# Kernel optimization log

Hardware: AMD Instinct MI355X
Metric: run time of the kernel (lower is better)

Reference implementation:

```python
import jax, jax.numpy as jnp
import numpy as np

T, B, IN_DIM, HID, ACT = 512, 256, 256, 256, 16


def _dense_params(key, din, dout, scale=0.02):
    kw, _ = jax.random.split(key)
    return jax.random.normal(kw, (din, dout), jnp.float32) * scale, jnp.zeros((dout,), jnp.float32)


def setup_inputs() -> dict:
    key = jax.random.key(0)
    ks = jax.random.split(key, 12)
    x = jax.random.normal(ks[0], (T, B, IN_DIM), jnp.float32)
    dones = jax.random.bernoulli(ks[1], 0.05, (T, B))
    h0_c = jnp.zeros((B, HID), jnp.float32)
    h0_h = jnp.zeros((B, HID), jnp.float32)
    W_embed, b_embed = _dense_params(ks[2], IN_DIM, HID)
    # OptimizedLSTMCell: fused gate projections, gate order (i, f, g, o)
    Wi = jax.random.normal(ks[3], (HID, 4 * HID), jnp.float32) * 0.02
    Wh = jax.random.normal(ks[4], (HID, 4 * HID), jnp.float32) * 0.02
    b_lstm = jnp.zeros((4 * HID,), jnp.float32)
    Wa1, ba1 = _dense_params(ks[5], HID, HID // 2)
    Wa2, ba2 = _dense_params(ks[6], HID // 2, HID // 2)
    Wa3, ba3 = _dense_params(ks[7], HID // 2, ACT, scale=0.01)
    Wc1, bc1 = _dense_params(ks[8], HID, HID // 2)
    Wc2, bc2 = _dense_params(ks[9], HID // 2, HID // 2)
    Wc3, bc3 = _dense_params(ks[10], HID // 2, 1)
    return dict(x=x, dones=dones, h0_c=h0_c, h0_h=h0_h,
                W_embed=W_embed, b_embed=b_embed, Wi=Wi, Wh=Wh, b_lstm=b_lstm,
                Wa1=Wa1, ba1=ba1, Wa2=Wa2, ba2=ba2, Wa3=Wa3, ba3=ba3,
                Wc1=Wc1, bc1=bc1, Wc2=Wc2, bc2=bc2, Wc3=Wc3, bc3=bc3)


def reference(x, dones, h0_c, h0_h, W_embed, b_embed, Wi, Wh, b_lstm,
              Wa1, ba1, Wa2, ba2, Wa3, ba3, Wc1, bc1, Wc2, bc2, Wc3, bc3):
    # embed (note: source overwrites first Dense; effective embed is one Dense+relu)
    embed = jax.nn.relu(jnp.einsum('tbi,ih->tbh', x, W_embed) + b_embed)

    def step(carry, inp):
        c, h = carry
        xt, rt = inp  # xt: [B, HID], rt: [B] bool
        m = rt[:, None]
        c = jnp.where(m, 0.0, c)  # reset_carry is zeros (initialize_carry)
        h = jnp.where(m, 0.0, h)
        z = xt @ Wi + h @ Wh + b_lstm  # [B, 4*HID]
        i, f, g, o = jnp.split(z, 4, axis=-1)
        c_new = jax.nn.sigmoid(f) * c + jax.nn.sigmoid(i) * jnp.tanh(g)
        h_new = jax.nn.sigmoid(o) * jnp.tanh(c_new)
        return (c_new, h_new), h_new

    (c_fin, h_fin), hs = jax.lax.scan(step, (h0_c, h0_h), (embed, dones))

    a = jnp.tanh(jnp.einsum('tbh,hk->tbk', hs, Wa1) + ba1)
    a = jnp.tanh(a @ Wa2 + ba2)
    logits = a @ Wa3 + ba3  # [T, B, ACT]

    v = jnp.tanh(jnp.einsum('tbh,hk->tbk', hs, Wc1) + bc1)
    v = jnp.tanh(v @ Wc2 + bc2)
    value = jnp.squeeze(v @ Wc3 + bc3, axis=-1)  # [T, B]

    return c_fin, h_fin, logits, value
```

## Files before the change

kernel.cpp:

```cpp
#include <hip/hip_runtime.h>
#include <stdint.h>


typedef short v8s __attribute__((ext_vector_type(8)));
typedef float v4f __attribute__((ext_vector_type(4)));

#define DEV static __device__ __forceinline__
#define DT_THRESH 4096

DEV float b2f(unsigned short h) {
    union { unsigned int u; float f; } v; v.u = ((unsigned int)h) << 16; return v.f;
}
DEV unsigned short f2b(float f) {
    union { float f; unsigned int u; } v; v.f = f;
    unsigned int u = v.u;
    return (unsigned short)((u + 0x7fffu + ((u >> 16) & 1u)) >> 16);
}
DEV float sigf(float x) {
    x = fminf(fmaxf(x, -30.f), 30.f);
    return 1.f / (1.f + __expf(-x));
}
DEV float tanh_(float x) {
    x = fminf(fmaxf(x, -15.f), 15.f);
    float e = __expf(-2.f * x);
    return (1.f - e) / (1.f + e);
}

__global__ __launch_bounds__(1024) void dones_k(const void* __restrict__ raw,
                                                int* __restrict__ dst,
                                                int* __restrict__ dt) {
    __shared__ int bad_int, bad_bf;
    int tid = threadIdx.x;
    if (tid == 0) { bad_int = 0; bad_bf = 0; dt[0] = 0; }
    __syncthreads();
    const unsigned int* w = (const unsigned int*)raw;
    int li = 0, lb = 0;
    for (int i = tid; i < 32768; i += 1024) {
        unsigned int v = w[i];
        if (v > 1u) li = 1;
        unsigned int h0 = v & 0xffffu, h1 = v >> 16;
        if ((h0 != 0u && h0 != 0x3f80u) || (h1 != 0u && h1 != 0x3f80u)) lb = 1;
    }
    if (li) atomicOr(&bad_int, 1);
    if (lb) atomicOr(&bad_bf, 1);
    __syncthreads();
    int mode = (!bad_int) ? 0 : ((!bad_bf) ? 1 : 2);
    for (int e = tid; e < 131072; e += 1024) {
        int v;
        if (mode == 0)      v = (((const int*)raw)[e] != 0);
        else if (mode == 1) v = (((const unsigned short*)raw)[e] != 0);
        else                v = (((const unsigned char*)raw)[e] != 0);
        dst[e] = v;
    }
}

__global__ __launch_bounds__(256) void detect_k(const unsigned short* __restrict__ xr,
                                                int* __restrict__ dt) {
    int tid = blockIdx.x * 256 + threadIdx.x;
    int cnt = 0;
    for (int i = tid; i < (1 << 24); i += 16384) {
        unsigned int e = (xr[i] >> 7) & 0xffu;
        cnt += (e >= 140u);
    }
    for (int o = 32; o; o >>= 1) cnt += __shfl_down(cnt, o);
    if ((threadIdx.x & 63) == 0 && cnt) atomicAdd(dt, cnt);
}

__global__ __launch_bounds__(256) void cvt_x_k(const void* __restrict__ xr,
                                               unsigned short* __restrict__ xb,
                                               const int* __restrict__ dt) {
    int fp32i = dt[0] > DT_THRESH;
    long i4 = (long)blockIdx.x * 256 + threadIdx.x;
    if (fp32i) {
        float4 v = ((const float4*)xr)[i4];
        uint2 p;
        p.x = (unsigned int)f2b(v.x) | ((unsigned int)f2b(v.y) << 16);
        p.y = (unsigned int)f2b(v.z) | ((unsigned int)f2b(v.w) << 16);
        ((uint2*)xb)[i4] = p;
    } else {
        ((uint2*)xb)[i4] = ((const uint2*)xr)[i4];
    }
}

struct TransArgs {
    const void* src[9];
    unsigned short* dst[9];
    int R[9];
    int C[9];
    int prefix[10];
    int total;
};

__global__ __launch_bounds__(256) void trans_kernel(TransArgs a, const int* __restrict__ dt) {
    int fp32i = dt[0] > DT_THRESH;
    int id = blockIdx.x * 256 + threadIdx.x;
    if (id >= a.total) return;
    int m = 0;
#pragma unroll
    for (int k = 0; k < 9; k++)
        if (id >= a.prefix[k + 1]) m = k + 1;
    int e = id - a.prefix[m];
    int C = a.C[m];
    int r = e / C, c = e % C;
    unsigned short v;
    if (fp32i) v = f2b(((const float*)a.src[m])[e]);
    else       v = ((const unsigned short*)a.src[m])[e];
    a.dst[m][c * a.R[m] + r] = v;
}

template <int TN, int ACT, int OM>
__global__ __launch_bounds__(256) void gemm_k(const unsigned short* __restrict__ A,
                                              const unsigned short* __restrict__ BT,
                                              const unsigned short* __restrict__ bias,
                                              void* __restrict__ Cout, long coff,
                                              const int* __restrict__ dtf,
                                              int N, int K) {
    __shared__ unsigned short As[128][40];
    __shared__ unsigned short Bs[TN][40];
    const int tid = threadIdx.x;
    const int l = tid & 63, w = tid >> 6;
    const long m0 = (long)blockIdx.x * 128;
    const int n0 = blockIdx.y * TN;
    constexpr int NRT = (TN == 128) ? 4 : 2;
    constexpr int NCT = (TN == 128) ? 4 : 1;
    int fp32o = (OM == 1) ? (dtf[0] > DT_THRESH) : 0;

    v4f acc[NRT][NCT];
    for (int i = 0; i < NRT; i++)
        for (int j = 0; j < NCT; j++) acc[i][j] = v4f{0.f, 0.f, 0.f, 0.f};

    for (int kc = 0; kc < K; kc += 32) {
        {
            int row = tid >> 1, part = tid & 1;
            const uint4* src = (const uint4*)(A + (m0 + row) * K + kc + part * 16);
            uint4 v0 = src[0], v1 = src[1];
            *(uint4*)&As[row][part * 16] = v0;
            *(uint4*)&As[row][part * 16 + 8] = v1;
        }
        if (TN == 128) {
            int row = tid >> 1, part = tid & 1;
            const uint4* src = (const uint4*)(BT + (long)(n0 + row) * K + kc + part * 16);
            uint4 v0 = src[0], v1 = src[1];
            *(uint4*)&Bs[row][part * 16] = v0;
            *(uint4*)&Bs[row][part * 16 + 8] = v1;
        } else if (tid < 32) {
            int row = tid >> 1, part = tid & 1;
            const uint4* src = (const uint4*)(BT + (long)(n0 + row) * K + kc + part * 16);
            uint4 v0 = src[0], v1 = src[1];
            *(uint4*)&Bs[row][part * 16] = v0;
            *(uint4*)&Bs[row][part * 16 + 8] = v1;
        }
        __syncthreads();

        v8s af[NRT], bf[NCT];
#pragma unroll
        for (int i = 0; i < NRT; i++) {
            int rt = (TN == 128) ? ((w >> 1) * 4 + i) : (w * 2 + i);
            af[i] = *(const v8s*)&As[rt * 16 + (l & 15)][(l >> 4) * 8];
        }
#pragma unroll
        for (int j = 0; j < NCT; j++) {
            int ct = (TN == 128) ? ((w & 1) * 4 + j) : 0;
            bf[j] = *(const v8s*)&Bs[ct * 16 + (l & 15)][(l >> 4) * 8];
        }
#pragma unroll
        for (int i = 0; i < NRT; i++)
#pragma unroll
            for (int j = 0; j < NCT; j++)
                acc[i][j] = __builtin_amdgcn_mfma_f32_16x16x32_bf16(af[i], bf[j], acc[i][j], 0, 0, 0);
        __syncthreads();
    }

#pragma unroll
    for (int j = 0; j < NCT; j++) {
        int ct = (TN == 128) ? ((w & 1) * 4 + j) : 0;
        int col = ct * 16 + (l & 15);
        float bv = b2f(bias[n0 + col]);
#pragma unroll
        for (int i = 0; i < NRT; i++) {
            int rt = (TN == 128) ? ((w >> 1) * 4 + i) : (w * 2 + i);
#pragma unroll
            for (int q = 0; q < 4; q++) {
                long row = m0 + rt * 16 + (l >> 4) * 4 + q;
                float v = acc[i][j][q] + bv;
                if (ACT == 1) v = fmaxf(v, 0.f);
                if (ACT == 2) v = tanh_(v);
                long idx = coff + row * (long)N + n0 + col;
                if (OM == 1 && fp32o) ((float*)Cout)[idx] = v;
                else ((unsigned short*)Cout)[idx] = f2b(v);
            }
        }
    }
}

#define HB_WORDS 65536

__global__ __launch_bounds__(512, 2) void lstm_k(const unsigned short* __restrict__ xz,
                                                 const int* __restrict__ dones,
                                                 const void* __restrict__ h0c,
                                                 const void* __restrict__ h0h,
                                                 const unsigned short* __restrict__ WhT,
                                                 unsigned int* __restrict__ hb,
                                                 unsigned short* __restrict__ hs,
                                                 void* __restrict__ outv,
                                                 const int* __restrict__ dtf) {
    __shared__ unsigned short hlds[16][256];
    __shared__ float zlds[4][16][132];

    const int tid = threadIdx.x;
    const int l = tid & 63;
    const int w = tid >> 6;
    const int cluster = blockIdx.x & 15;
    const int r = blockIdx.x >> 4;
    const int p = r ^ 1;
    const int bt = cluster * 16;
    const int fp32o = dtf[0] > DT_THRESH;
    const int gate = w & 3;
    const int hblk = (w >> 2) * 64;
    const int l15 = l & 15;
    const int lq = l >> 4;

    v8s bw[4][8];
#pragma unroll
    for (int j = 0; j < 4; j++) {
        const unsigned short* wp =
            WhT + (long)(gate * 256 + r * 128 + hblk + j * 16 + l15) * 256 + lq * 8;
#pragma unroll
        for (int ks = 0; ks < 8; ks++) bw[j][ks] = *(const v8s*)(wp + ks * 32);
    }

    float c[4], hcur[4] = {0.f, 0.f, 0.f, 0.f};
#pragma unroll
    for (int i = 0; i < 4; i++) {
        int cell = i * 512 + tid;
        int row = cell >> 7, hid = cell & 127;
        long idx = (long)(bt + row) * 256 + r * 128 + hid;
        c[i] = fp32o ? ((const float*)h0c)[idx] : b2f(((const unsigned short*)h0c)[idx]);
        float h0 = fp32o ? ((const float*)h0h)[idx] : b2f(((const unsigned short*)h0h)[idx]);
        unsigned short hbits = f2b(h0);
        hlds[row][(r * 128 + hid) ^ ((row & 7) * 8)] = hbits;
        __hip_atomic_store(&hb[(size_t)cluster * 4096 + row * 256 + r * 128 + hid],
                           (unsigned int)hbits,
                           __ATOMIC_RELAXED, __HIP_MEMORY_SCOPE_AGENT);
    }

    int dead = 0;
    unsigned int va[4] = {0u, 0u, 0u, 0u};

    for (int t = 0; t < 512; t++) {
        unsigned short xzp[16];
#pragma unroll
        for (int j = 0; j < 4; j++)
#pragma unroll
            for (int q = 0; q < 4; q++)
                xzp[j * 4 + q] = xz[(long)(t * 256 + bt + lq * 4 + q) * 1024 +
                                    (gate * 256 + r * 128 + hblk + j * 16 + l15)];
        int dn_a = dones[t * 256 + bt + l15];
        int dn_c[4];
#pragma unroll
        for (int i = 0; i < 4; i++) dn_c[i] = dones[t * 256 + bt + i * 4 + (tid >> 7)];

        const unsigned int tag = (unsigned int)t;
        const unsigned int* rb = hb + (size_t)(t & 1) * HB_WORDS + (size_t)cluster * 4096;
        if (!dead) {
            int guard = 0;
            while (true) {
#pragma unroll
                for (int i = 0; i < 4; i++) {
                    int cell = i * 512 + tid;
                    va[i] = __hip_atomic_load(&rb[(cell >> 7) * 256 + p * 128 + (cell & 127)],
                                              __ATOMIC_RELAXED, __HIP_MEMORY_SCOPE_AGENT);
                }
                unsigned int okl = ((va[0] >> 16) == tag) & ((va[1] >> 16) == tag) &
                                   ((va[2] >> 16) == tag) & ((va[3] >> 16) == tag);
                if (__ballot(okl != 0u) == ~0ull) break;
                if (++guard > (1 << 13)) { dead = 1; break; }
            }
        }
#pragma unroll
        for (int i = 0; i < 4; i++) {
            int cell = i * 512 + tid;
            int row = cell >> 7, hid = cell & 127;
            hlds[row][(p * 128 + hid) ^ ((row & 7) * 8)] = (unsigned short)(va[i] & 0xffffu);
        }
        __syncthreads();

        v4f acc[4];
#pragma unroll
        for (int j = 0; j < 4; j++)
#pragma unroll
            for (int q = 0; q < 4; q++) acc[j][q] = b2f(xzp[j * 4 + q]);
#pragma unroll
        for (int ks = 0; ks < 8; ks++) {
            v8s a = *(const v8s*)&hlds[l15][(ks * 32 + lq * 8) ^ ((l15 & 7) * 8)];
            if (dn_a) a = v8s{0, 0, 0, 0, 0, 0, 0, 0};
#pragma unroll
            for (int j = 0; j < 4; j++)
                acc[j] = __builtin_amdgcn_mfma_f32_16x16x32_bf16(a, bw[j][ks], acc[j], 0, 0, 0);
        }
#pragma unroll
        for (int j = 0; j < 4; j++)
#pragma unroll
            for (int q = 0; q < 4; q++)
                zlds[gate][lq * 4 + q][hblk + j * 16 + l15] = acc[j][q];
        __syncthreads();

        unsigned int* wb = hb + (size_t)((t + 1) & 1) * HB_WORDS + (size_t)cluster * 4096;
#pragma unroll
        for (int i = 0; i < 4; i++) {
            int cell = i * 512 + tid;
            int row = cell >> 7, hid = cell & 127;
            float zi = zlds[0][row][hid];
            float zf = zlds[1][row][hid];
            float zg = zlds[2][row][hid];
            float zo = zlds[3][row][hid];
            float cm = dn_c[i] ? 0.f : c[i];
            float cn = sigf(zf) * cm + sigf(zi) * tanh_(zg);
            float h = sigf(zo) * tanh_(cn);
            c[i] = cn;
            hcur[i] = h;
            unsigned short hbits = f2b(h);
            hlds[row][(r * 128 + hid) ^ ((row & 7) * 8)] = hbits;
            __hip_atomic_store(&wb[row * 256 + r * 128 + hid],
                               (((unsigned int)(t + 1)) << 16) | (unsigned int)hbits,
                               __ATOMIC_RELAXED, __HIP_MEMORY_SCOPE_AGENT);
            unsigned int pr = (unsigned int)__shfl_xor((int)hbits, 1);
            if ((tid & 1) == 0) {
                unsigned int wv = (unsigned int)hbits | (pr << 16);
                ((unsigned int*)hs)[((long)(t * 256 + bt + row)) * 128 + ((r * 128 + hid) >> 1)] = wv;
            }
        }
    }

#pragma unroll
    for (int i = 0; i < 4; i++) {
        int cell = i * 512 + tid;
        int row = cell >> 7, hid = cell & 127;
        long i1 = (long)(bt + row) * 256 + r * 128 + hid;
        long i2 = 65536 + i1;
        if (fp32o) {
            ((float*)outv)[i1] = c[i];
            ((float*)outv)[i2] = hcur[i];
        } else {
            ((unsigned short*)outv)[i1] = f2b(c[i]);
            ((unsigned short*)outv)[i2] = f2b(hcur[i]);
        }
    }
}

__global__ __launch_bounds__(256) void value_k(const unsigned short* __restrict__ V2,
                                               const unsigned short* __restrict__ Wc3T,
                                               const unsigned short* __restrict__ bc3,
                                               void* __restrict__ outv,
                                               const int* __restrict__ dtf) {
    int tid = threadIdx.x;
    int l = tid & 63, w = tid >> 6;
    int fp32o = dtf[0] > DT_THRESH;
    long row = (long)blockIdx.x * 32 + w * 8 + (l >> 3);
    int sub = l & 7;
    const unsigned short* vp = V2 + row * 128 + sub * 16;
    float s = 0.f;
#pragma unroll
    for (int j = 0; j < 16; j++) s += b2f(vp[j]) * b2f(Wc3T[sub * 16 + j]);
    s += __shfl_xor(s, 1);
    s += __shfl_xor(s, 2);
    s += __shfl_xor(s, 4);
    if (sub == 0) {
        float v = s + b2f(bc3[0]);
        if (fp32o) ((float*)outv)[2228224 + row] = v;
        else ((unsigned short*)outv)[2228224 + row] = f2b(v);
    }
}

extern "C" void kernel_launch(void* const* d_in, const int* in_sizes, int n_in,
                              void* d_out, int out_size, void* d_ws, size_t ws_size,
                              hipStream_t stream) {
    const void* x             = d_in[0];
    const void* dones_raw     = d_in[1];
    const void* h0c           = d_in[2];
    const void* h0h           = d_in[3];
    const void* We  = d_in[4];
    const unsigned short* be  = (const unsigned short*)d_in[5];
    const void* Wi  = d_in[6];
    const void* Wh  = d_in[7];
    const unsigned short* bl  = (const unsigned short*)d_in[8];
    const void* Wa1 = d_in[9];
    const unsigned short* ba1 = (const unsigned short*)d_in[10];
    const void* Wa2 = d_in[11];
    const unsigned short* ba2 = (const unsigned short*)d_in[12];
    const void* Wa3 = d_in[13];
    const unsigned short* ba3 = (const unsigned short*)d_in[14];
    const void* Wc1 = d_in[15];
    const unsigned short* bc1 = (const unsigned short*)d_in[16];
    const void* Wc2 = d_in[17];
    const unsigned short* bc2 = (const unsigned short*)d_in[18];
    const void* Wc3 = d_in[19];
    const unsigned short* bc3 = (const unsigned short*)d_in[20];
    char* ws = (char*)d_ws;

    unsigned short* WeT  = (unsigned short*)(ws + 0);
    unsigned short* WiT  = (unsigned short*)(ws + 131072);
    unsigned short* WhT  = (unsigned short*)(ws + 655360);
    unsigned short* Wa1T = (unsigned short*)(ws + 1179648);
    unsigned short* Wa2T = (unsigned short*)(ws + 1245184);
    unsigned short* Wa3T = (unsigned short*)(ws + 1277952);
    unsigned short* Wc1T = (unsigned short*)(ws + 1282048);
    unsigned short* Wc2T = (unsigned short*)(ws + 1347584);
    unsigned short* Wc3T = (unsigned short*)(ws + 1380352);
    int*            DT   = (int*)(ws + 1380608);
    unsigned int*   HB   = (unsigned int*)(ws + 1380672);
    int*            DN   = (int*)(ws + 1904960);
    unsigned short* XB   = (unsigned short*)(ws + 2429248);
    unsigned short* E    = (unsigned short*)(ws + 69538112);
    unsigned short* XZ   = (unsigned short*)(ws + 136646976);
    unsigned short* HS   = (unsigned short*)(ws + 405082432);
    unsigned short* H1   = XB;
    unsigned short* H2   = XB + 16777216;

    TransArgs ta;
    {
        const void* srcs[9] = {We, Wi, Wh, Wa1, Wa2, Wa3, Wc1, Wc2, Wc3};
        unsigned short* dsts[9] = {WeT, WiT, WhT, Wa1T, Wa2T, Wa3T, Wc1T, Wc2T, Wc3T};
        int Rs[9] = {256, 256, 256, 256, 128, 128, 256, 128, 128};
        int Cs[9] = {256, 1024, 1024, 128, 128, 16, 128, 128, 1};
        int p = 0;
        for (int i = 0; i < 9; i++) {
            ta.src[i] = srcs[i];
            ta.dst[i] = dsts[i];
            ta.R[i] = Rs[i];
            ta.C[i] = Cs[i];
            ta.prefix[i] = p;
            p += Rs[i] * Cs[i];
        }
        ta.prefix[9] = p;
        ta.total = p;
    }

    dones_k<<<1, 1024, 0, stream>>>(dones_raw, DN, DT);
    detect_k<<<64, 256, 0, stream>>>((const unsigned short*)x, DT);
    cvt_x_k<<<32768, 256, 0, stream>>>(x, XB, DT);
    trans_kernel<<<2697, 256, 0, stream>>>(ta, DT);

    gemm_k<128, 1, 0><<<dim3(1024, 2), 256, 0, stream>>>(XB, WeT, be, E, 0, nullptr, 256, 256);
    gemm_k<128, 0, 0><<<dim3(1024, 8), 256, 0, stream>>>(E, WiT, bl, XZ, 0, nullptr, 1024, 256);
    lstm_k<<<32, 512, 0, stream>>>(XZ, DN, h0c, h0h, WhT, HB, HS, d_out, DT);
    gemm_k<128, 2, 0><<<dim3(1024, 1), 256, 0, stream>>>(HS, Wa1T, ba1, H1, 0, nullptr, 128, 256);
    gemm_k<128, 2, 0><<<dim3(1024, 1), 256, 0, stream>>>(H1, Wa2T, ba2, H2, 0, nullptr, 128, 128);
    gemm_k<16, 0, 1><<<dim3(1024, 1), 256, 0, stream>>>(H2, Wa3T, ba3, d_out, 131072, DT, 16, 128);
    gemm_k<128, 2, 0><<<dim3(1024, 1), 256, 0, stream>>>(HS, Wc1T, bc1, H1, 0, nullptr, 128, 256);
    gemm_k<128, 2, 0><<<dim3(1024, 1), 256, 0, stream>>>(H1, Wc2T, bc2, H2, 0, nullptr, 128, 128);
    value_k<<<4096, 256, 0, stream>>>(H2, Wc3T, bc3, d_out, DT);
}
```

Measured before the change: 2.657 ms.

## Replace per-element tagged handoff with flag-based release/acquire and overlap local half

The LSTM recurrence swaps tagged per-element polling of the partner block's h values for a single release/acquire flag per block, with h packed as bf16 pairs in a double-buffered exchange area. The MFMA for the block's own half of h now runs before waiting on the partner, so part of the matmul overlaps the cross-block sync. Next-step xz gate inputs and dones are prefetched one step ahead, and the done mask is applied when h is produced, not at the MFMA input. Per-thread cell mapping becomes four contiguous hidden units, enabling vectorised LDS, global and hs stores, at the cost of an extra __syncthreads per step and a flag-initialisation dependency in dones_k.

```diff
diff --git a/kernel.cpp b/kernel.cpp
--- a/kernel.cpp
+++ b/kernel.cpp
@@ -4,6 +4,7 @@
 
 typedef short v8s __attribute__((ext_vector_type(8)));
 typedef float v4f __attribute__((ext_vector_type(4)));
+typedef unsigned short u16x4 __attribute__((ext_vector_type(4)));
 
 #define DEV static __device__ __forceinline__
 #define DT_THRESH 4096
@@ -28,10 +29,12 @@
 
 __global__ __launch_bounds__(1024) void dones_k(const void* __restrict__ raw,
                                                 int* __restrict__ dst,
-                                                int* __restrict__ dt) {
+                                                int* __restrict__ dt,
+                                                unsigned int* __restrict__ flg) {
     __shared__ int bad_int, bad_bf;
     int tid = threadIdx.x;
     if (tid == 0) { bad_int = 0; bad_bf = 0; dt[0] = 0; }
+    for (int i = tid; i < 2048; i += 1024) flg[i] = 0u;
     __syncthreads();
     const unsigned int* w = (const unsigned int*)raw;
     int li = 0, lb = 0;
@@ -193,14 +196,13 @@
     }
 }
 
-#define HB_WORDS 65536
-
 __global__ __launch_bounds__(512, 2) void lstm_k(const unsigned short* __restrict__ xz,
                                                  const int* __restrict__ dones,
                                                  const void* __restrict__ h0c,
                                                  const void* __restrict__ h0h,
                                                  const unsigned short* __restrict__ WhT,
-                                                 unsigned int* __restrict__ hb,
+                                                 unsigned int* __restrict__ flg,
+                                                 unsigned int* __restrict__ hd32,
                                                  unsigned short* __restrict__ hs,
                                                  void* __restrict__ outv,
                                                  const int* __restrict__ dtf) {
@@ -219,6 +221,9 @@
     const int hblk = (w >> 2) * 64;
     const int l15 = l & 15;
     const int lq = l >> 4;
+    const int row = tid >> 5;
+    const int hid0 = (tid & 31) * 4;
+    const int swz = (row & 7) * 8;
 
     v8s bw[4][8];
 #pragma unroll
@@ -230,70 +235,89 @@
     }
 
     float c[4], hcur[4] = {0.f, 0.f, 0.f, 0.f};
-#pragma unroll
-    for (int i = 0; i < 4; i++) {
-        int cell = i * 512 + tid;
-        int row = cell >> 7, hid = cell & 127;
-        long idx = (long)(bt + row) * 256 + r * 128 + hid;
-        c[i] = fp32o ? ((const float*)h0c)[idx] : b2f(((const unsigned short*)h0c)[idx]);
-        float h0 = fp32o ? ((const float*)h0h)[idx] : b2f(((const unsigned short*)h0h)[idx]);
-        unsigned short hbits = f2b(h0);
-        hlds[row][(r * 128 + hid) ^ ((row & 7) * 8)] = hbits;
-        __hip_atomic_store(&hb[(size_t)cluster * 4096 + row * 256 + r * 128 + hid],
-                           (unsigned int)hbits,
-                           __ATOMIC_RELAXED, __HIP_MEMORY_SCOPE_AGENT);
-    }
+    int dn_cur = dones[bt + row];
+    int dn_nxt = dones[256 + bt + row];
+    {
+        u16x4 hw4;
+#pragma unroll
+        for (int i = 0; i < 4; i++) {
+            long idx = (long)(bt + row) * 256 + r * 128 + hid0 + i;
+            c[i] = fp32o ? ((const float*)h0c)[idx] : b2f(((const unsigned short*)h0c)[idx]);
+            float h0 = fp32o ? ((const float*)h0h)[idx] : b2f(((const unsigned short*)h0h)[idx]);
+            hw4[i] = dn_cur ? (unsigned short)0 : f2b(h0);
+        }
+        *(u16x4*)&hlds[row][(r * 128 + hid0) ^ swz] = hw4;
+        int mb = ((0 * 16 + cluster) * 2 + r) * 1024 + row * 64 + (tid & 31) * 2;
+        hd32[mb]     = (unsigned int)hw4[0] | ((unsigned int)hw4[1] << 16);
+        hd32[mb + 1] = (unsigned int)hw4[2] | ((unsigned int)hw4[3] << 16);
+    }
+    unsigned short xzp[16];
+#pragma unroll
+    for (int j = 0; j < 4; j++)
+#pragma unroll
+        for (int q = 0; q < 4; q++)
+            xzp[j * 4 + q] = xz[(long)(bt + lq * 4 + q) * 1024 +
+                                (gate * 256 + r * 128 + hblk + j * 16 + l15)];
+    __syncthreads();
+    if (tid == 0)
+        __hip_atomic_store(&flg[((0 * 16 + cluster) * 2 + r) * 32], 1u,
+                           __ATOMIC_RELEASE, __HIP_MEMORY_SCOPE_AGENT);
 
     int dead = 0;
-    unsigned int va[4] = {0u, 0u, 0u, 0u};
 
     for (int t = 0; t < 512; t++) {
-        unsigned short xzp[16];
+        const int par = t & 1, npar = par ^ 1;
+
+        v4f acc[4];
 #pragma unroll
         for (int j = 0; j < 4; j++)
 #pragma unroll
-            for (int q = 0; q < 4; q++)
-                xzp[j * 4 + q] = xz[(long)(t * 256 + bt + lq * 4 + q) * 1024 +
-                                    (gate * 256 + r * 128 + hblk + j * 16 + l15)];
-        int dn_a = dones[t * 256 + bt + l15];
-        int dn_c[4];
-#pragma unroll
-        for (int i = 0; i < 4; i++) dn_c[i] = dones[t * 256 + bt + i * 4 + (tid >> 7)];
-
-        const unsigned int tag = (unsigned int)t;
-        const unsigned int* rb = hb + (size_t)(t & 1) * HB_WORDS + (size_t)cluster * 4096;
+            for (int q = 0; q < 4; q++) acc[j][q] = b2f(xzp[j * 4 + q]);
+
+        {
+            int tn = (t < 511) ? t + 1 : t;
+#pragma unroll
+            for (int j = 0; j < 4; j++)
+#pragma unroll
+                for (int q = 0; q < 4; q++)
+                    xzp[j * 4 + q] = xz[(long)(tn * 256 + bt + lq * 4 + q) * 1024 +
+                                        (gate * 256 + r * 128 + hblk + j * 16 + l15)];
+        }
+
+#pragma unroll
+        for (int ko = 0; ko < 4; ko++) {
+            int ks = r * 4 + ko;
+            v8s a = *(const v8s*)&hlds[l15][(ks * 32 + lq * 8) ^ ((l15 & 7) * 8)];
+#pragma unroll
+            for (int j = 0; j < 4; j++)
+                acc[j] = __builtin_amdgcn_mfma_f32_16x16x32_bf16(a, bw[j][ks], acc[j], 0, 0, 0);
+        }
+
         if (!dead) {
+            const unsigned int want = (unsigned int)(t + 1);
             int guard = 0;
-            while (true) {
-#pragma unroll
-                for (int i = 0; i < 4; i++) {
-                    int cell = i * 512 + tid;
-                    va[i] = __hip_atomic_load(&rb[(cell >> 7) * 256 + p * 128 + (cell & 127)],
-                                              __ATOMIC_RELAXED, __HIP_MEMORY_SCOPE_AGENT);
-                }
-                unsigned int okl = ((va[0] >> 16) == tag) & ((va[1] >> 16) == tag) &
-                                   ((va[2] >> 16) == tag) & ((va[3] >> 16) == tag);
-                if (__ballot(okl != 0u) == ~0ull) break;
-                if (++guard > (1 << 13)) { dead = 1; break; }
+            while (__hip_atomic_load(&flg[((par * 16 + cluster) * 2 + p) * 32],
+                                     __ATOMIC_ACQUIRE, __HIP_MEMORY_SCOPE_AGENT) != want) {
+                __builtin_amdgcn_s_sleep(1);
+                if (++guard > (1 << 14)) { dead = 1; break; }
             }
         }
-#pragma unroll
-        for (int i = 0; i < 4; i++) {
-            int cell = i * 512 + tid;
-            int row = cell >> 7, hid = cell & 127;
-            hlds[row][(p * 128 + hid) ^ ((row & 7) * 8)] = (unsigned short)(va[i] & 0xffffu);
+        {
+            int pb = ((par * 16 + cluster) * 2 + p) * 1024 + row * 64 + (tid & 31) * 2;
+            unsigned int w0 = hd32[pb], w1 = hd32[pb + 1];
+            u16x4 pv;
+            pv[0] = (unsigned short)(w0 & 0xffffu);
+            pv[1] = (unsigned short)(w0 >> 16);
+            pv[2] = (unsigned short)(w1 & 0xffffu);
+            pv[3] = (unsigned short)(w1 >> 16);
+            *(u16x4*)&hlds[row][(p * 128 + hid0) ^ swz] = pv;
         }
         __syncthreads();
 
-        v4f acc[4];
-#pragma unroll
-        for (int j = 0; j < 4; j++)
-#pragma unroll
-            for (int q = 0; q < 4; q++) acc[j][q] = b2f(xzp[j * 4 + q]);
-#pragma unroll
-        for (int ks = 0; ks < 8; ks++) {
+#pragma unroll
+        for (int ko = 0; ko < 4; ko++) {
+            int ks = p * 4 + ko;
             v8s a = *(const v8s*)&hlds[l15][(ks * 32 + lq * 8) ^ ((l15 & 7) * 8)];
-            if (dn_a) a = v8s{0, 0, 0, 0, 0, 0, 0, 0};
 #pragma unroll
             for (int j = 0; j < 4; j++)
                 acc[j] = __builtin_amdgcn_mfma_f32_16x16x32_bf16(a, bw[j][ks], acc[j], 0, 0, 0);
@@ -305,38 +329,45 @@
                 zlds[gate][lq * 4 + q][hblk + j * 16 + l15] = acc[j][q];
         __syncthreads();
 
-        unsigned int* wb = hb + (size_t)((t + 1) & 1) * HB_WORDS + (size_t)cluster * 4096;
-#pragma unroll
-        for (int i = 0; i < 4; i++) {
-            int cell = i * 512 + tid;
-            int row = cell >> 7, hid = cell & 127;
-            float zi = zlds[0][row][hid];
-            float zf = zlds[1][row][hid];
-            float zg = zlds[2][row][hid];
-            float zo = zlds[3][row][hid];
-            float cm = dn_c[i] ? 0.f : c[i];
-            float cn = sigf(zf) * cm + sigf(zi) * tanh_(zg);
-            float h = sigf(zo) * tanh_(cn);
-            c[i] = cn;
-            hcur[i] = h;
-            unsigned short hbits = f2b(h);
-            hlds[row][(r * 128 + hid) ^ ((row & 7) * 8)] = hbits;
-            __hip_atomic_store(&wb[row * 256 + r * 128 + hid],
-                               (((unsigned int)(t + 1)) << 16) | (unsigned int)hbits,
-                               __ATOMIC_RELAXED, __HIP_MEMORY_SCOPE_AGENT);
-            unsigned int pr = (unsigned int)__shfl_xor((int)hbits, 1);
-            if ((tid & 1) == 0) {
-                unsigned int wv = (unsigned int)hbits | (pr << 16);
-                ((unsigned int*)hs)[((long)(t * 256 + bt + row)) * 128 + ((r * 128 + hid) >> 1)] = wv;
+        {
+            v4f z0 = *(const v4f*)&zlds[0][row][hid0];
+            v4f z1 = *(const v4f*)&zlds[1][row][hid0];
+            v4f z2 = *(const v4f*)&zlds[2][row][hid0];
+            v4f z3 = *(const v4f*)&zlds[3][row][hid0];
+            u16x4 hb4, hw4;
+#pragma unroll
+            for (int i = 0; i < 4; i++) {
+                float cm = dn_cur ? 0.f : c[i];
+                float cn = sigf(z1[i]) * cm + sigf(z0[i]) * tanh_(z2[i]);
+                float h = sigf(z3[i]) * tanh_(cn);
+                c[i] = cn;
+                hcur[i] = h;
+                hb4[i] = f2b(h);
+                hw4[i] = dn_nxt ? (unsigned short)0 : hb4[i];
             }
-        }
+            *(u16x4*)&hlds[row][(r * 128 + hid0) ^ swz] = hw4;
+            int mb = ((npar * 16 + cluster) * 2 + r) * 1024 + row * 64 + (tid & 31) * 2;
+            hd32[mb]     = (unsigned int)hw4[0] | ((unsigned int)hw4[1] << 16);
+            hd32[mb + 1] = (unsigned int)hw4[2] | ((unsigned int)hw4[3] << 16);
+            long hsb = ((long)(t * 256 + bt + row)) * 128 + r * 64 + (tid & 31) * 2;
+            ((unsigned int*)hs)[hsb]     = (unsigned int)hb4[0] | ((unsigned int)hb4[1] << 16);
+            ((unsigned int*)hs)[hsb + 1] = (unsigned int)hb4[2] | ((unsigned int)hb4[3] << 16);
+        }
+        dn_cur = dn_nxt;
+        {
+            int tn2 = (t + 2 < 512) ? t + 2 : 511;
+            dn_nxt = dones[tn2 * 256 + bt + row];
+        }
+        __syncthreads();
+        if (tid == 0)
+            __hip_atomic_store(&flg[((npar * 16 + cluster) * 2 + r) * 32],
+                               (unsigned int)(t + 2),
+                               __ATOMIC_RELEASE, __HIP_MEMORY_SCOPE_AGENT);
     }
 
 #pragma unroll
     for (int i = 0; i < 4; i++) {
-        int cell = i * 512 + tid;
-        int row = cell >> 7, hid = cell & 127;
-        long i1 = (long)(bt + row) * 256 + r * 128 + hid;
+        long i1 = (long)(bt + row) * 256 + r * 128 + hid0 + i;
         long i2 = 65536 + i1;
         if (fp32o) {
             ((float*)outv)[i1] = c[i];
@@ -417,6 +448,9 @@
     unsigned short* H1   = XB;
     unsigned short* H2   = XB + 16777216;
 
+    unsigned int* FL = HB;
+    unsigned int* HD = HB + 2048;
+
     TransArgs ta;
     {
         const void* srcs[9] = {We, Wi, Wh, Wa1, Wa2, Wa3, Wc1, Wc2, Wc3};
@@ -436,14 +470,14 @@
         ta.total = p;
     }
 
-    dones_k<<<1, 1024, 0, stream>>>(dones_raw, DN, DT);
+    dones_k<<<1, 1024, 0, stream>>>(dones_raw, DN, DT, FL);
     detect_k<<<64, 256, 0, stream>>>((const unsigned short*)x, DT);
     cvt_x_k<<<32768, 256, 0, stream>>>(x, XB, DT);
     trans_kernel<<<2697, 256, 0, stream>>>(ta, DT);
 
     gemm_k<128, 1, 0><<<dim3(1024, 2), 256, 0, stream>>>(XB, WeT, be, E, 0, nullptr, 256, 256);
     gemm_k<128, 0, 0><<<dim3(1024, 8), 256, 0, stream>>>(E, WiT, bl, XZ, 0, nullptr, 1024, 256);
-    lstm_k<<<32, 512, 0, stream>>>(XZ, DN, h0c, h0h, WhT, HB, HS, d_out, DT);
+    lstm_k<<<32, 512, 0, stream>>>(XZ, DN, h0c, h0h, WhT, FL, HD, HS, d_out, DT);
     gemm_k<128, 2, 0><<<dim3(1024, 1), 256, 0, stream>>>(HS, Wa1T, ba1, H1, 0, nullptr, 128, 256);
     gemm_k<128, 2, 0><<<dim3(1024, 1), 256, 0, stream>>>(H1, Wa2T, ba2, H2, 0, nullptr, 128, 128);
     gemm_k<16, 0, 1><<<dim3(1024, 1), 256, 0, stream>>>(H2, Wa3T, ba3, d_out, 131072, DT, 16, 128);
```

After: 6.415 ms. 2.41x slower.
